# Kernel tuning notes

Measured on AMD Instinct MI355X. Metric: run time of the kernel, lower is better.

The kernel has to match this reference:

```python
import jax, jax.numpy as jnp
import numpy as np

B, T, F = 32, 500, 640   # batch, encoder frames, encoder feature dim
H = 640                  # prediction-net LSTM hidden
J = 640                  # joint dim
V = 1024                 # vocab size
BLANK = 0                # blank_id


def setup_inputs() -> dict:
    key = jax.random.key(0)
    ks = jax.random.split(key, 8)
    s = 0.02
    return {
        "tn_output": jax.random.normal(ks[0], (B, T, F), jnp.float32),
        "E": jax.random.normal(ks[1], (V, H), jnp.float32) * s,        # prediction-net embedding
        "W_ih": jax.random.normal(ks[2], (H, 4 * H), jnp.float32) * s,  # LSTM input weights
        "W_hh": jax.random.normal(ks[3], (H, 4 * H), jnp.float32) * s,  # LSTM recurrent weights
        "b_lstm": jnp.zeros((4 * H,), jnp.float32),
        "W_enc": jax.random.normal(ks[4], (F, J), jnp.float32) * s,     # joint: encoder projection
        "W_dec": jax.random.normal(ks[5], (H, J), jnp.float32) * s,     # joint: decoder projection
        "b_j": jnp.zeros((J,), jnp.float32),
        "W_out": jax.random.normal(ks[6], (J, V), jnp.float32) * s,     # joint: output projection
        "b_out": jnp.zeros((V,), jnp.float32),
    }


def _lstm_step(x, h, c, W_ih, W_hh, b):
    gates = x @ W_ih + h @ W_hh + b  # [B, 4H]
    i, f, g, o = jnp.split(gates, 4, axis=-1)
    c2 = jax.nn.sigmoid(f) * c + jax.nn.sigmoid(i) * jnp.tanh(g)
    h2 = jax.nn.sigmoid(o) * jnp.tanh(c2)
    return h2, c2


def _greedy_decode(tn_output, E, W_ih, W_hh, b_lstm, W_enc, W_dec, b_j, W_out, b_out):
    Bc = tn_output.shape[0]
    dt = tn_output.dtype
    tok0 = jnp.full((Bc,), BLANK, jnp.int32)
    h0 = jnp.zeros((Bc, H), dt)
    c0 = jnp.zeros((Bc, H), dt)
    # initial decoder call on blank token (hidden=None -> zeros)
    h1, c1 = _lstm_step(E[tok0], h0, c0, W_ih, W_hh, b_lstm)
    g0 = h1  # out_PN

    def step(carry, enc_t):
        h, c, g, last_tok, scores = carry
        # joint network + log_softmax (idempotent, applied once)
        logits = jnp.tanh(enc_t @ W_enc + g @ W_dec + b_j) @ W_out + b_out  # [B, V]
        logp = jax.nn.log_softmax(logits, axis=-1)
        tok = jnp.argmax(logp, axis=-1)                                     # [B]
        lp = jnp.take_along_axis(logp, tok[:, None], axis=1)[:, 0]          # logp_targets
        emit = tok != BLANK                                                 # [B] bool
        scores = scores + jnp.where(emit, lp, jnp.zeros_like(lp))
        new_tok = jnp.where(emit, tok.astype(jnp.int32), last_tok)
        # conditional decoder step: run LSTM on all rows, keep updates only where emit
        h2, c2 = _lstm_step(E[new_tok], h, c, W_ih, W_hh, b_lstm)
        m = emit[:, None]
        h = jnp.where(m, h2, h)
        c = jnp.where(m, c2, c)
        g = jnp.where(m, h2, g)
        out_tok = jnp.where(emit, tok.astype(jnp.int32), jnp.int32(BLANK))
        return (h, c, g, new_tok, scores), out_tok

    init = (h1, c1, g0, tok0, jnp.zeros((Bc,), dt))
    (_, _, _, _, scores), toks = jax.lax.scan(step, init, jnp.swapaxes(tn_output, 0, 1))
    return jnp.swapaxes(toks, 0, 1), scores  # [B,T] int tokens (BLANK = no emission), [B] logp scores


def reference(tn_output, E, W_ih, W_hh, b_lstm, W_enc, W_dec, b_j, W_out, b_out):
    toks, scores = _greedy_decode(tn_output, E, W_ih, W_hh, b_lstm, W_enc, W_dec, b_j, W_out, b_out)
    # original returns (predictions, mean of exp(logp_scores), None, None)
    return toks, jnp.exp(scores).mean()
```

## Files before the change

### kernel.cpp

```cpp
#include <hip/hip_runtime.h>
#include <math.h>

#define BB 32
#define TT 500
#define HH 640
#define VV 1024
#define NWG 256


__device__ __forceinline__ float sigf(float x) { return 1.0f / (1.0f + expf(-x)); }

__device__ __forceinline__ unsigned int fkey(float x) {
    unsigned int u = __float_as_uint(x);
    return (u & 0x80000000u) ? ~u : (u | 0x80000000u);
}

__device__ __forceinline__ unsigned long long shflxor_u64(unsigned long long v, int m) {
    unsigned int lo = (unsigned int)v, hi = (unsigned int)(v >> 32);
    lo = (unsigned int)__shfl_xor((int)lo, m);
    hi = (unsigned int)__shfl_xor((int)hi, m);
    return ((unsigned long long)hi << 32) | lo;
}

__device__ __forceinline__ void gbar(unsigned int* arrive, unsigned int* release,
                                     int w, int tid, unsigned int k) {
    __syncthreads();
    if (w == 0) {
        if (tid > 0) {
            while (__hip_atomic_load(&arrive[tid * 32], __ATOMIC_RELAXED,
                                     __HIP_MEMORY_SCOPE_AGENT) < k)
                __builtin_amdgcn_s_sleep(2);
        }
        __syncthreads();
        __threadfence();
        if (tid > 0)
            __hip_atomic_store(&release[tid * 32], k, __ATOMIC_RELAXED,
                               __HIP_MEMORY_SCOPE_AGENT);
        __syncthreads();
    } else {
        if (tid == 0) {
            __threadfence();
            __hip_atomic_store(&arrive[w * 32], k, __ATOMIC_RELAXED,
                               __HIP_MEMORY_SCOPE_AGENT);
            while (__hip_atomic_load(&release[w * 32], __ATOMIC_RELAXED,
                                     __HIP_MEMORY_SCOPE_AGENT) < k)
                __builtin_amdgcn_s_sleep(2);
            __threadfence();
        }
        __syncthreads();
    }
}

__global__ __launch_bounds__(256) void gemm_bias_kernel(
    const float* __restrict__ A, const float* __restrict__ Bm,
    const float* __restrict__ bias, float* __restrict__ C,
    int M, int N, int K)
{
    __shared__ float As[16][65];
    __shared__ float Bs[16][64];
    int tid = threadIdx.x;
    int m0 = blockIdx.y * 64, n0 = blockIdx.x * 64;
    int ar = tid >> 2, ac = (tid & 3) * 4;
    int br4 = (tid >> 6) * 4, bc = tid & 63;
    int ty = tid >> 4, tx = tid & 15;
    float acc[4][4] = {};
    for (int k0 = 0; k0 < K; k0 += 16) {
        float4 av = *(const float4*)(A + (long)(m0 + ar) * K + k0 + ac);
        As[ac + 0][ar] = av.x; As[ac + 1][ar] = av.y;
        As[ac + 2][ar] = av.z; As[ac + 3][ar] = av.w;
#pragma unroll
        for (int i = 0; i < 4; ++i)
            Bs[br4 + i][bc] = Bm[(long)(k0 + br4 + i) * N + n0 + bc];
        __syncthreads();
#pragma unroll
        for (int kk = 0; kk < 16; ++kk) {
            float a[4], b[4];
#pragma unroll
            for (int i = 0; i < 4; ++i) a[i] = As[kk][ty * 4 + i];
#pragma unroll
            for (int j = 0; j < 4; ++j) b[j] = Bs[kk][tx * 4 + j];
#pragma unroll
            for (int i = 0; i < 4; ++i)
#pragma unroll
                for (int j = 0; j < 4; ++j)
                    acc[i][j] = fmaf(a[i], b[j], acc[i][j]);
        }
        __syncthreads();
    }
#pragma unroll
    for (int i = 0; i < 4; ++i)
#pragma unroll
        for (int j = 0; j < 4; ++j)
            C[(long)(m0 + ty * 4 + i) * N + n0 + tx * 4 + j] =
                acc[i][j] + bias[n0 + tx * 4 + j];
}

__global__ void init_kernel(const float* __restrict__ EW, float* __restrict__ h,
                            float* __restrict__ c, float* __restrict__ scores,
                            unsigned int* __restrict__ arrive,
                            unsigned int* __restrict__ release)
{
    int tid = threadIdx.x;
    for (int j = tid; j < HH; j += 256) {
        float gi = EW[j], gg = EW[1280 + j], go = EW[1920 + j];
        float c1 = sigf(gi) * tanhf(gg);
        float h1 = sigf(go) * tanhf(c1);
        for (int b = 0; b < BB; ++b) { h[b * 640 + j] = h1; c[b * 640 + j] = c1; }
    }
    if (tid < 32) scores[tid] = 0.f;
    arrive[tid * 32] = 0u;
    release[tid * 32] = 0u;
}

__global__ __launch_bounds__(256, 1) void decode_kernel(
    const float* __restrict__ ENC, const float* __restrict__ EW,
    const float* __restrict__ Wdec, const float* __restrict__ Whh,
    const float* __restrict__ Wout, const float* __restrict__ bout,
    float* __restrict__ h, float* __restrict__ c,
    float* __restrict__ Tt, float* __restrict__ G,
    unsigned long long* __restrict__ pmax, float* __restrict__ psum,
    float* __restrict__ scores, float* __restrict__ out,
    unsigned int* arrive, unsigned int* release)
{
    __shared__ float Wa[640 * 16];
    __shared__ float Wo[640 * 4];
    __shared__ unsigned long long red_m[4];
    __shared__ float red_s[4];
    __shared__ int s_tok, s_emit;

    int w = blockIdx.x, tid = threadIdx.x;

    if (w < 200) {
        if (w < 40) {
            const float* src = Wdec + w * 16;
            for (int i = tid; i < 640 * 16; i += 256) {
                int k = i >> 4, cc = i & 15;
                Wa[i] = src[k * 640 + cc];
            }
        } else {
            const float* src = Whh + (w * 16 - 640);
            for (int i = tid; i < 640 * 16; i += 256) {
                int k = i >> 4, cc = i & 15;
                Wa[i] = src[k * 2560 + cc];
            }
        }
    }
    {
        const float* src = Wout + w * 4;
        for (int i = tid; i < 640 * 4; i += 256) {
            int k = i >> 2, cc = i & 3;
            Wo[i] = src[k * 1024 + cc];
        }
    }
    __syncthreads();

    unsigned int bk = 0;

    for (int t = 0; t < TT; ++t) {
        if (w < 200) {
            int b = tid >> 3, cg = tid & 7;
            int lc = cg * 2;
            const float* hb = h + b * 640;
            float a0 = 0.f, a1 = 0.f;
            for (int k0 = 0; k0 < 640; k0 += 4) {
                float4 hv = *(const float4*)(hb + k0);
                float hl[4] = {hv.x, hv.y, hv.z, hv.w};
#pragma unroll
                for (int j = 0; j < 4; ++j) {
                    float2 wv = *(const float2*)(&Wa[(k0 + j) * 16 + lc]);
                    a0 = fmaf(hl[j], wv.x, a0);
                    a1 = fmaf(hl[j], wv.y, a1);
                }
            }
            int gc = w * 16 + lc;
            if (gc < 640) {
                const float* e = ENC + ((long)b * TT + t) * 640;
                Tt[b * 640 + gc]     = tanhf(e[gc] + a0);
                Tt[b * 640 + gc + 1] = tanhf(e[gc + 1] + a1);
            } else {
                G[b * 2560 + gc - 640]     = a0;
                G[b * 2560 + gc - 640 + 1] = a1;
            }
        }
        gbar(arrive, release, w, tid, ++bk);

        {
            int half = tid & 1, p = tid >> 1, b = p >> 2, cl = p & 3;
            const float* tb = Tt + b * 640 + half * 320;
            const float* wb = Wo + half * 1280 + cl;
            float acc = 0.f;
            for (int k0 = 0; k0 < 320; k0 += 4) {
                float4 tv = *(const float4*)(tb + k0);
                acc = fmaf(tv.x, wb[(k0 + 0) * 4], acc);
                acc = fmaf(tv.y, wb[(k0 + 1) * 4], acc);
                acc = fmaf(tv.z, wb[(k0 + 2) * 4], acc);
                acc = fmaf(tv.w, wb[(k0 + 3) * 4], acc);
            }
            float oth = __shfl_xor(acc, 1);
            int col = w * 4 + cl;
            float logit = acc + oth + bout[col];
            float sexp = expf(logit);
            unsigned long long pk =
                ((unsigned long long)fkey(logit) << 32) | (unsigned int)(1023 - col);
            unsigned long long o;
            o = shflxor_u64(pk, 2); if (o > pk) pk = o; sexp += __shfl_xor(sexp, 2);
            o = shflxor_u64(pk, 4); if (o > pk) pk = o; sexp += __shfl_xor(sexp, 4);
            if ((tid & 7) == 0) {
                pmax[b * 256 + w] = pk;
                psum[b * 256 + w] = sexp;
            }
        }
        gbar(arrive, release, w, tid, ++bk);

        if (w < 32) {
            int b = w;
            unsigned long long m = pmax[b * 256 + tid];
            float s = psum[b * 256 + tid];
#pragma unroll
            for (int mask = 1; mask <= 32; mask <<= 1) {
                unsigned long long o = shflxor_u64(m, mask);
                if (o > m) m = o;
                s += __shfl_xor(s, mask);
            }
            if ((tid & 63) == 0) { red_m[tid >> 6] = m; red_s[tid >> 6] = s; }
            __syncthreads();
            if (tid == 0) {
                unsigned long long mm = red_m[0];
                float ss = red_s[0];
#pragma unroll
                for (int i = 1; i < 4; ++i) {
                    if (red_m[i] > mm) mm = red_m[i];
                    ss += red_s[i];
                }
                int tok = 1023 - (int)(mm & 0xFFFFFFFFu);
                unsigned int key = (unsigned int)(mm >> 32);
                unsigned int u = (key & 0x80000000u) ? (key ^ 0x80000000u) : ~key;
                float maxlogit = __uint_as_float(u);
                int emit = (tok != 0);
                out[b * TT + t] = (float)tok;
                if (emit) scores[b] += maxlogit - logf(ss);
                s_tok = tok; s_emit = emit;
            }
            __syncthreads();
            if (s_emit) {
                const float* ew = EW + (long)s_tok * 2560;
                const float* gb = G + b * 2560;
                for (int j = tid; j < 640; j += 256) {
                    float gi = ew[j] + gb[j];
                    float gf = ew[640 + j] + gb[640 + j];
                    float gg = ew[1280 + j] + gb[1280 + j];
                    float go = ew[1920 + j] + gb[1920 + j];
                    float cn = sigf(gf) * c[b * 640 + j] + sigf(gi) * tanhf(gg);
                    float hn = sigf(go) * tanhf(cn);
                    c[b * 640 + j] = cn;
                    h[b * 640 + j] = hn;
                }
            }
        }
        gbar(arrive, release, w, tid, ++bk);
    }

    if (w == 0 && tid == 0) {
        float s = 0.f;
        for (int b = 0; b < 32; ++b) s += expf(scores[b]);
        out[16000] = s / 32.0f;
    }
}

extern "C" void kernel_launch(void* const* d_in, const int* in_sizes, int n_in,
                              void* d_out, int out_size, void* d_ws, size_t ws_size,
                              hipStream_t stream)
{
    const float* X     = (const float*)d_in[0];
    const float* E     = (const float*)d_in[1];
    const float* W_ih  = (const float*)d_in[2];
    const float* W_hh  = (const float*)d_in[3];
    const float* b_l   = (const float*)d_in[4];
    const float* W_enc = (const float*)d_in[5];
    const float* W_dec = (const float*)d_in[6];
    const float* b_j   = (const float*)d_in[7];
    const float* W_out = (const float*)d_in[8];
    const float* b_out = (const float*)d_in[9];

    float* ws  = (float*)d_ws;
    float* ENC = ws;
    float* EW  = ws + 10240000;
    float* h   = ws + 12861440;
    float* c   = ws + 12881920;
    float* Tt  = ws + 12902400;
    float* G   = ws + 12922880;
    unsigned long long* pmax = (unsigned long long*)(ws + 13004800);
    float* psum   = ws + 13021184;
    float* scores = ws + 13029376;
    unsigned int* arrive  = (unsigned int*)(ws + 13029440);
    unsigned int* release = (unsigned int*)(ws + 13037632);
    float* out = (float*)d_out;

    gemm_bias_kernel<<<dim3(10, 250), 256, 0, stream>>>(X, W_enc, b_j, ENC, 16000, 640, 640);
    gemm_bias_kernel<<<dim3(40, 16), 256, 0, stream>>>(E, W_ih, b_l, EW, 1024, 2560, 640);
    init_kernel<<<1, 256, 0, stream>>>(EW, h, c, scores, arrive, release);

    void* args[] = {
        (void*)&ENC, (void*)&EW, (void*)&W_dec, (void*)&W_hh,
        (void*)&W_out, (void*)&b_out, (void*)&h, (void*)&c,
        (void*)&Tt, (void*)&G, (void*)&pmax, (void*)&psum,
        (void*)&scores, (void*)&out, (void*)&arrive, (void*)&release
    };
    hipLaunchCooperativeKernel((const void*)decode_kernel, dim3(NWG), dim3(256),
                               args, 0, stream);
}
```

Baseline: 25.06 ms.

## Replace barrier fences with cache-bypassing stores/loads and stage activations in LDS

Removes the __threadfence calls from the grid barrier and instead writes and reads cross-workgroup data (Tt, G, h, pmax, psum, scores) with sc0 sc1 global stores and loads, waiting on vmcnt before each barrier. The recurrent and output matvecs now stage h and Tt rows into dynamic LDS, use a transposed, padded weight layout, and split the K dimension across four groups with an LDS reduction. The LSTM update is vectorised to float4, and per-batch scores are kept in registers until the end. This targets the per-step barrier latency and global memory reads in the 500-step serial loop, at the cost of relying on inline-asm cache coherence semantics and a large dynamic LDS allocation.

After: 32.23 ms. 1.29x slower.

```diff
diff --git a/kernel.cpp b/kernel.cpp
--- a/kernel.cpp
+++ b/kernel.cpp
@@ -7,6 +7,10 @@
 #define VV 1024
 #define NWG 256
 
+typedef float f32x4 __attribute__((ext_vector_type(4)));
+typedef float f32x2 __attribute__((ext_vector_type(2)));
+typedef unsigned int u32x2 __attribute__((ext_vector_type(2)));
+
 
 __device__ __forceinline__ float sigf(float x) { return 1.0f / (1.0f + expf(-x)); }
 
@@ -22,30 +26,74 @@
     return ((unsigned long long)hi << 32) | lo;
 }
 
+__device__ __forceinline__ void stg1_sc(float* p, float v) {
+    asm volatile("global_store_dword %0, %1, off sc0 sc1" :: "v"(p), "v"(v) : "memory");
+}
+__device__ __forceinline__ void stg2_sc(float* p, f32x2 v) {
+    asm volatile("global_store_dwordx2 %0, %1, off sc0 sc1" :: "v"(p), "v"(v) : "memory");
+}
+__device__ __forceinline__ void stg4_sc(float* p, f32x4 v) {
+    asm volatile("global_store_dwordx4 %0, %1, off sc0 sc1" :: "v"(p), "v"(v) : "memory");
+}
+__device__ __forceinline__ void stg2u_sc(unsigned long long* p, unsigned long long v) {
+    u32x2 uv; uv.x = (unsigned int)v; uv.y = (unsigned int)(v >> 32);
+    asm volatile("global_store_dwordx2 %0, %1, off sc0 sc1" :: "v"(p), "v"(uv) : "memory");
+}
+
+__device__ __forceinline__ void stage_rows(const float* src, float* dst) {
+    f32x4 t0,t1,t2,t3,t4,t5,t6,t7,t8,t9,t10,t11,t12,t13,t14,t15,t16,t17,t18,t19;
+    asm volatile(
+        "global_load_dwordx4 %0,  %20, off sc0 sc1\n\t"
+        "global_load_dwordx4 %1,  %20, off offset:16 sc0 sc1\n\t"
+        "global_load_dwordx4 %2,  %20, off offset:32 sc0 sc1\n\t"
+        "global_load_dwordx4 %3,  %20, off offset:48 sc0 sc1\n\t"
+        "global_load_dwordx4 %4,  %20, off offset:64 sc0 sc1\n\t"
+        "global_load_dwordx4 %5,  %20, off offset:80 sc0 sc1\n\t"
+        "global_load_dwordx4 %6,  %20, off offset:96 sc0 sc1\n\t"
+        "global_load_dwordx4 %7,  %20, off offset:112 sc0 sc1\n\t"
+        "global_load_dwordx4 %8,  %20, off offset:128 sc0 sc1\n\t"
+        "global_load_dwordx4 %9,  %20, off offset:144 sc0 sc1\n\t"
+        "global_load_dwordx4 %10, %20, off offset:160 sc0 sc1\n\t"
+        "global_load_dwordx4 %11, %20, off offset:176 sc0 sc1\n\t"
+        "global_load_dwordx4 %12, %20, off offset:192 sc0 sc1\n\t"
+        "global_load_dwordx4 %13, %20, off offset:208 sc0 sc1\n\t"
+        "global_load_dwordx4 %14, %20, off offset:224 sc0 sc1\n\t"
+        "global_load_dwordx4 %15, %20, off offset:240 sc0 sc1\n\t"
+        "global_load_dwordx4 %16, %20, off offset:256 sc0 sc1\n\t"
+        "global_load_dwordx4 %17, %20, off offset:272 sc0 sc1\n\t"
+        "global_load_dwordx4 %18, %20, off offset:288 sc0 sc1\n\t"
+        "global_load_dwordx4 %19, %20, off offset:304 sc0 sc1\n\t"
+        "s_waitcnt vmcnt(0)"
+        : "=&v"(t0),"=&v"(t1),"=&v"(t2),"=&v"(t3),"=&v"(t4),"=&v"(t5),"=&v"(t6),"=&v"(t7),
+          "=&v"(t8),"=&v"(t9),"=&v"(t10),"=&v"(t11),"=&v"(t12),"=&v"(t13),"=&v"(t14),"=&v"(t15),
+          "=&v"(t16),"=&v"(t17),"=&v"(t18),"=&v"(t19)
+        : "v"(src) : "memory");
+    f32x4* d = (f32x4*)dst;
+    d[0]=t0; d[1]=t1; d[2]=t2; d[3]=t3; d[4]=t4; d[5]=t5; d[6]=t6; d[7]=t7;
+    d[8]=t8; d[9]=t9; d[10]=t10; d[11]=t11; d[12]=t12; d[13]=t13; d[14]=t14;
+    d[15]=t15; d[16]=t16; d[17]=t17; d[18]=t18; d[19]=t19;
+}
+
 __device__ __forceinline__ void gbar(unsigned int* arrive, unsigned int* release,
                                      int w, int tid, unsigned int k) {
+    asm volatile("s_waitcnt vmcnt(0)" ::: "memory");
     __syncthreads();
     if (w == 0) {
-        if (tid > 0) {
+        if (tid > 0)
             while (__hip_atomic_load(&arrive[tid * 32], __ATOMIC_RELAXED,
                                      __HIP_MEMORY_SCOPE_AGENT) < k)
                 __builtin_amdgcn_s_sleep(2);
-        }
         __syncthreads();
-        __threadfence();
         if (tid > 0)
             __hip_atomic_store(&release[tid * 32], k, __ATOMIC_RELAXED,
                                __HIP_MEMORY_SCOPE_AGENT);
-        __syncthreads();
     } else {
         if (tid == 0) {
-            __threadfence();
             __hip_atomic_store(&arrive[w * 32], k, __ATOMIC_RELAXED,
                                __HIP_MEMORY_SCOPE_AGENT);
             while (__hip_atomic_load(&release[w * 32], __ATOMIC_RELAXED,
                                      __HIP_MEMORY_SCOPE_AGENT) < k)
                 __builtin_amdgcn_s_sleep(2);
-            __threadfence();
         }
         __syncthreads();
     }
@@ -112,6 +160,8 @@
     release[tid * 32] = 0u;
 }
 
+extern __shared__ float lds[];
+
 __global__ __launch_bounds__(256, 1) void decode_kernel(
     const float* __restrict__ ENC, const float* __restrict__ EW,
     const float* __restrict__ Wdec, const float* __restrict__ Whh,
@@ -122,8 +172,10 @@
     float* __restrict__ scores, float* __restrict__ out,
     unsigned int* arrive, unsigned int* release)
 {
-    __shared__ float Wa[640 * 16];
-    __shared__ float Wo[640 * 4];
+    float* Wa = lds;
+    float* Wo = lds + 10304;
+    float* S  = lds + 12880;
+    float* P  = lds + 33488;
     __shared__ unsigned long long red_m[4];
     __shared__ float red_s[4];
     __shared__ int s_tok, s_emit;
@@ -131,70 +183,94 @@
     int w = blockIdx.x, tid = threadIdx.x;
 
     if (w < 200) {
-        if (w < 40) {
-            const float* src = Wdec + w * 16;
-            for (int i = tid; i < 640 * 16; i += 256) {
-                int k = i >> 4, cc = i & 15;
-                Wa[i] = src[k * 640 + cc];
-            }
-        } else {
-            const float* src = Whh + (w * 16 - 640);
-            for (int i = tid; i < 640 * 16; i += 256) {
-                int k = i >> 4, cc = i & 15;
-                Wa[i] = src[k * 2560 + cc];
-            }
-        }
+        int cc = tid >> 4, k0 = (tid & 15) * 40;
+        const float* src; long stride;
+        if (w < 40) { src = Wdec + (w * 16 + cc); stride = 640; }
+        else        { src = Whh + (w * 16 - 640 + cc); stride = 2560; }
+        for (int i = 0; i < 40; ++i)
+            Wa[cc * 644 + k0 + i] = src[(long)(k0 + i) * stride];
     }
     {
-        const float* src = Wout + w * 4;
-        for (int i = tid; i < 640 * 4; i += 256) {
-            int k = i >> 2, cc = i & 3;
-            Wo[i] = src[k * 1024 + cc];
-        }
+        int cc = tid >> 6, k0 = (tid & 63) * 10;
+        const float* src = Wout + (w * 4 + cc);
+        for (int i = 0; i < 10; ++i)
+            Wo[cc * 644 + k0 + i] = src[(long)(k0 + i) * 1024];
     }
     __syncthreads();
 
+    int srow = tid >> 3, scol = (tid & 7) * 80;
+    float score = 0.f;
     unsigned int bk = 0;
 
     for (int t = 0; t < TT; ++t) {
         if (w < 200) {
-            int b = tid >> 3, cg = tid & 7;
+            stage_rows(h + srow * 640 + scol, &S[srow * 644 + scol]);
+            __syncthreads();
+            int ks = tid >> 6, bg = (tid >> 3) & 7, cg = tid & 7;
             int lc = cg * 2;
-            const float* hb = h + b * 640;
-            float a0 = 0.f, a1 = 0.f;
-            for (int k0 = 0; k0 < 640; k0 += 4) {
-                float4 hv = *(const float4*)(hb + k0);
-                float hl[4] = {hv.x, hv.y, hv.z, hv.w};
-#pragma unroll
-                for (int j = 0; j < 4; ++j) {
-                    float2 wv = *(const float2*)(&Wa[(k0 + j) * 16 + lc]);
-                    a0 = fmaf(hl[j], wv.x, a0);
-                    a1 = fmaf(hl[j], wv.y, a1);
-                }
-            }
-            int gc = w * 16 + lc;
+            const float* wa0 = &Wa[lc * 644];
+            const float* wa1 = &Wa[(lc + 1) * 644];
+            const float* sp0 = &S[(4 * bg + 0) * 644];
+            const float* sp1 = &S[(4 * bg + 1) * 644];
+            const float* sp2 = &S[(4 * bg + 2) * 644];
+            const float* sp3 = &S[(4 * bg + 3) * 644];
+            float a00=0,a01=0,a10=0,a11=0,a20=0,a21=0,a30=0,a31=0;
+            int kend = ks * 160 + 160;
+            for (int k0 = ks * 160; k0 < kend; k0 += 4) {
+                float4 w0 = *(const float4*)(wa0 + k0);
+                float4 w1 = *(const float4*)(wa1 + k0);
+                float4 h0 = *(const float4*)(sp0 + k0);
+                float4 h1 = *(const float4*)(sp1 + k0);
+                float4 h2 = *(const float4*)(sp2 + k0);
+                float4 h3 = *(const float4*)(sp3 + k0);
+                a00=fmaf(h0.x,w0.x,a00); a00=fmaf(h0.y,w0.y,a00); a00=fmaf(h0.z,w0.z,a00); a00=fmaf(h0.w,w0.w,a00);
+                a01=fmaf(h0.x,w1.x,a01); a01=fmaf(h0.y,w1.y,a01); a01=fmaf(h0.z,w1.z,a01); a01=fmaf(h0.w,w1.w,a01);
+                a10=fmaf(h1.x,w0.x,a10); a10=fmaf(h1.y,w0.y,a10); a10=fmaf(h1.z,w0.z,a10); a10=fmaf(h1.w,w0.w,a10);
+                a11=fmaf(h1.x,w1.x,a11); a11=fmaf(h1.y,w1.y,a11); a11=fmaf(h1.z,w1.z,a11); a11=fmaf(h1.w,w1.w,a11);
+                a20=fmaf(h2.x,w0.x,a20); a20=fmaf(h2.y,w0.y,a20); a20=fmaf(h2.z,w0.z,a20); a20=fmaf(h2.w,w0.w,a20);
+                a21=fmaf(h2.x,w1.x,a21); a21=fmaf(h2.y,w1.y,a21); a21=fmaf(h2.z,w1.z,a21); a21=fmaf(h2.w,w1.w,a21);
+                a30=fmaf(h3.x,w0.x,a30); a30=fmaf(h3.y,w0.y,a30); a30=fmaf(h3.z,w0.z,a30); a30=fmaf(h3.w,w0.w,a30);
+                a31=fmaf(h3.x,w1.x,a31); a31=fmaf(h3.y,w1.y,a31); a31=fmaf(h3.z,w1.z,a31); a31=fmaf(h3.w,w1.w,a31);
+            }
+            f32x2 v;
+            v.x=a00; v.y=a01; *(f32x2*)&P[ks*580 + (4*bg+0)*18 + lc] = v;
+            v.x=a10; v.y=a11; *(f32x2*)&P[ks*580 + (4*bg+1)*18 + lc] = v;
+            v.x=a20; v.y=a21; *(f32x2*)&P[ks*580 + (4*bg+2)*18 + lc] = v;
+            v.x=a30; v.y=a31; *(f32x2*)&P[ks*580 + (4*bg+3)*18 + lc] = v;
+            __syncthreads();
+            int o0 = tid * 2, ob = o0 >> 4, oc = o0 & 15;
+            float r0 = 0.f, r1 = 0.f;
+#pragma unroll
+            for (int kr = 0; kr < 4; ++kr) {
+                f32x2 pv = *(const f32x2*)&P[kr*580 + ob*18 + oc];
+                r0 += pv.x; r1 += pv.y;
+            }
+            int gc = w * 16 + oc;
             if (gc < 640) {
-                const float* e = ENC + ((long)b * TT + t) * 640;
-                Tt[b * 640 + gc]     = tanhf(e[gc] + a0);
-                Tt[b * 640 + gc + 1] = tanhf(e[gc + 1] + a1);
+                float2 ev = *(const float2*)&ENC[((long)ob * TT + t) * 640 + gc];
+                f32x2 tv; tv.x = tanhf(ev.x + r0); tv.y = tanhf(ev.y + r1);
+                stg2_sc(&Tt[ob * 640 + gc], tv);
             } else {
-                G[b * 2560 + gc - 640]     = a0;
-                G[b * 2560 + gc - 640 + 1] = a1;
+                f32x2 gv; gv.x = r0; gv.y = r1;
+                stg2_sc(&G[ob * 2560 + gc - 640], gv);
             }
         }
         gbar(arrive, release, w, tid, ++bk);
 
+        stage_rows(Tt + srow * 640 + scol, &S[srow * 644 + scol]);
+        __syncthreads();
         {
-            int half = tid & 1, p = tid >> 1, b = p >> 2, cl = p & 3;
-            const float* tb = Tt + b * 640 + half * 320;
-            const float* wb = Wo + half * 1280 + cl;
+            int half = tid & 1, p2 = tid >> 1, bb = p2 >> 2, cl = p2 & 3;
+            const float* tb = &S[bb * 644 + half * 320];
+            const float* wb = &Wo[cl * 644 + half * 320];
             float acc = 0.f;
             for (int k0 = 0; k0 < 320; k0 += 4) {
                 float4 tv = *(const float4*)(tb + k0);
-                acc = fmaf(tv.x, wb[(k0 + 0) * 4], acc);
-                acc = fmaf(tv.y, wb[(k0 + 1) * 4], acc);
-                acc = fmaf(tv.z, wb[(k0 + 2) * 4], acc);
-                acc = fmaf(tv.w, wb[(k0 + 3) * 4], acc);
+                float4 wv = *(const float4*)(wb + k0);
+                acc = fmaf(tv.x, wv.x, acc);
+                acc = fmaf(tv.y, wv.y, acc);
+                acc = fmaf(tv.z, wv.z, acc);
+                acc = fmaf(tv.w, wv.w, acc);
             }
             float oth = __shfl_xor(acc, 1);
             int col = w * 4 + cl;
@@ -206,16 +282,23 @@
             o = shflxor_u64(pk, 2); if (o > pk) pk = o; sexp += __shfl_xor(sexp, 2);
             o = shflxor_u64(pk, 4); if (o > pk) pk = o; sexp += __shfl_xor(sexp, 4);
             if ((tid & 7) == 0) {
-                pmax[b * 256 + w] = pk;
-                psum[b * 256 + w] = sexp;
+                stg2u_sc(pmax + bb * 256 + w, pk);
+                stg1_sc(psum + bb * 256 + w, sexp);
             }
         }
         gbar(arrive, release, w, tid, ++bk);
 
         if (w < 32) {
             int b = w;
-            unsigned long long m = pmax[b * 256 + tid];
-            float s = psum[b * 256 + tid];
+            u32x2 mv; float s;
+            asm volatile(
+                "global_load_dwordx2 %0, %2, off sc0 sc1\n\t"
+                "global_load_dword   %1, %3, off sc0 sc1\n\t"
+                "s_waitcnt vmcnt(0)"
+                : "=&v"(mv), "=&v"(s)
+                : "v"(pmax + b * 256 + tid), "v"(psum + b * 256 + tid)
+                : "memory");
+            unsigned long long m = ((unsigned long long)mv.y << 32) | mv.x;
 #pragma unroll
             for (int mask = 1; mask <= 32; mask <<= 1) {
                 unsigned long long o = shflxor_u64(m, mask);
@@ -238,32 +321,73 @@
                 float maxlogit = __uint_as_float(u);
                 int emit = (tok != 0);
                 out[b * TT + t] = (float)tok;
-                if (emit) scores[b] += maxlogit - logf(ss);
+                if (emit) score += maxlogit - logf(ss);
                 s_tok = tok; s_emit = emit;
             }
             __syncthreads();
-            if (s_emit) {
-                const float* ew = EW + (long)s_tok * 2560;
-                const float* gb = G + b * 2560;
-                for (int j = tid; j < 640; j += 256) {
-                    float gi = ew[j] + gb[j];
-                    float gf = ew[640 + j] + gb[640 + j];
-                    float gg = ew[1280 + j] + gb[1280 + j];
-                    float go = ew[1920 + j] + gb[1920 + j];
-                    float cn = sigf(gf) * c[b * 640 + j] + sigf(gi) * tanhf(gg);
-                    float hn = sigf(go) * tanhf(cn);
-                    c[b * 640 + j] = cn;
-                    h[b * 640 + j] = hn;
-                }
+            if (s_emit && tid < 160) {
+                int j4 = tid * 4;
+                const float* gb = G + b * 2560 + j4;
+                f32x4 vi, vf, vg, vo;
+                asm volatile(
+                    "global_load_dwordx4 %0, %4, off sc0 sc1\n\t"
+                    "global_load_dwordx4 %1, %5, off sc0 sc1\n\t"
+                    "global_load_dwordx4 %2, %6, off sc0 sc1\n\t"
+                    "global_load_dwordx4 %3, %7, off sc0 sc1\n\t"
+                    "s_waitcnt vmcnt(0)"
+                    : "=&v"(vi), "=&v"(vf), "=&v"(vg), "=&v"(vo)
+                    : "v"(gb), "v"(gb + 640), "v"(gb + 1280), "v"(gb + 1920)
+                    : "memory");
+                const float* ew = EW + (long)s_tok * 2560 + j4;
+                float4 ei = *(const float4*)(ew);
+                float4 ef = *(const float4*)(ew + 640);
+                float4 eg = *(const float4*)(ew + 1280);
+                float4 eo = *(const float4*)(ew + 1920);
+                float4 cv = *(const float4*)(c + b * 640 + j4);
+                float4 cn; f32x4 hn;
+                cn.x = sigf(vf.x + ef.x) * cv.x + sigf(vi.x + ei.x) * tanhf(vg.x + eg.x);
+                cn.y = sigf(vf.y + ef.y) * cv.y + sigf(vi.y + ei.y) * tanhf(vg.y + eg.y);
+                cn.z = sigf(vf.z + ef.z) * cv.z + sigf(vi.z + ei.z) * tanhf(vg.z + eg.z);
+                cn.w = sigf(vf.w + ef.w) * cv.w + sigf(vi.w + ei.w) * tanhf(vg.w + eg.w);
+                hn.x = sigf(vo.x + eo.x) * tanhf(cn.x);
+                hn.y = sigf(vo.y + eo.y) * tanhf(cn.y);
+                hn.z = sigf(vo.z + eo.z) * tanhf(cn.z);
+                hn.w = sigf(vo.w + eo.w) * tanhf(cn.w);
+                *(float4*)(c + b * 640 + j4) = cn;
+                stg4_sc(h + b * 640 + j4, hn);
             }
         }
         gbar(arrive, release, w, tid, ++bk);
     }
 
+    if (w < 32 && tid == 0)
+        stg1_sc(scores + w, score);
+    gbar(arrive, release, w, tid, ++bk);
+
     if (w == 0 && tid == 0) {
-        float s = 0.f;
-        for (int b = 0; b < 32; ++b) s += expf(scores[b]);
-        out[16000] = s / 32.0f;
+        f32x4 s0,s1,s2,s3,s4,s5,s6,s7;
+        asm volatile(
+            "global_load_dwordx4 %0, %8, off sc0 sc1\n\t"
+            "global_load_dwordx4 %1, %8, off offset:16 sc0 sc1\n\t"
+            "global_load_dwordx4 %2, %8, off offset:32 sc0 sc1\n\t"
+            "global_load_dwordx4 %3, %8, off offset:48 sc0 sc1\n\t"
+            "global_load_dwordx4 %4, %8, off offset:64 sc0 sc1\n\t"
+            "global_load_dwordx4 %5, %8, off offset:80 sc0 sc1\n\t"
+            "global_load_dwordx4 %6, %8, off offset:96 sc0 sc1\n\t"
+            "global_load_dwordx4 %7, %8, off offset:112 sc0 sc1\n\t"
+            "s_waitcnt vmcnt(0)"
+            : "=&v"(s0),"=&v"(s1),"=&v"(s2),"=&v"(s3),
+              "=&v"(s4),"=&v"(s5),"=&v"(s6),"=&v"(s7)
+            : "v"(scores) : "memory");
+        float sum = expf(s0.x)+expf(s0.y)+expf(s0.z)+expf(s0.w)
+                  + expf(s1.x)+expf(s1.y)+expf(s1.z)+expf(s1.w)
+                  + expf(s2.x)+expf(s2.y)+expf(s2.z)+expf(s2.w)
+                  + expf(s3.x)+expf(s3.y)+expf(s3.z)+expf(s3.w)
+                  + expf(s4.x)+expf(s4.y)+expf(s4.z)+expf(s4.w)
+                  + expf(s5.x)+expf(s5.y)+expf(s5.z)+expf(s5.w)
+                  + expf(s6.x)+expf(s6.y)+expf(s6.z)+expf(s6.w)
+                  + expf(s7.x)+expf(s7.y)+expf(s7.z)+expf(s7.w);
+        out[16000] = sum / 32.0f;
     }
 }
 
@@ -307,5 +431,5 @@
         (void*)&scores, (void*)&out, (void*)&arrive, (void*)&release
     };
     hipLaunchCooperativeKernel((const void*)decode_kernel, dim3(NWG), dim3(256),
-                               args, 0, stream);
-}
+                               args, 143232, stream);
+}
```
